# Kernel tuning notes

Measured on AMD Instinct MI355X. Metric: run time of the kernel, lower is better.

The kernel has to match this reference:

```python
import jax, jax.numpy as jnp
import numpy as np

IN_DIM = 128
OUT_DIM = 256
N_ETYPES = 4
N_STEPS = 8
B = 128
N_NODES = 256
E = 393216
CONCAT = IN_DIM + OUT_DIM


def _conv1d(x, w, b):
    # x: [B, C, L], w: [O, I, K] -> valid conv, stride 1
    y = jax.lax.conv_general_dilated(x, w, (1,), 'VALID', dimension_numbers=('NCH', 'OIH', 'NCH'))
    return y + b[None, :, None]


def _maxpool1d(x, k, s):
    return jax.lax.reduce_window(x, -jnp.inf, jax.lax.max, (1, 1, k), (1, 1, s), 'VALID')


def setup_inputs():
    key = jax.random.key(0)
    ks = jax.random.split(key, 16)
    Nn = B * N_NODES
    sc = 0.05
    f32 = jnp.float32
    return {
        'features': jax.random.normal(ks[0], (Nn, IN_DIM), f32),
        'src': jax.random.randint(ks[1], (E,), 0, Nn),
        'dst': jax.random.randint(ks[2], (E,), 0, Nn),
        'etype': jax.random.randint(ks[3], (E,), 0, N_ETYPES),
        'W_msg': jax.random.normal(ks[4], (N_ETYPES, OUT_DIM, OUT_DIM), f32) * sc,
        'b_msg': jnp.zeros((N_ETYPES, OUT_DIM), f32),
        'gru_Wi': jax.random.normal(ks[5], (OUT_DIM, 3 * OUT_DIM), f32) * sc,
        'gru_Wh': jax.random.normal(ks[6], (OUT_DIM, 3 * OUT_DIM), f32) * sc,
        'gru_bi': jnp.zeros((3 * OUT_DIM,), f32),
        'gru_bh': jnp.zeros((3 * OUT_DIM,), f32),
        'conv1_w': jax.random.normal(ks[7], (OUT_DIM, OUT_DIM, 3), f32) * sc,
        'conv1_b': jnp.zeros((OUT_DIM,), f32),
        'conv2_w': jax.random.normal(ks[8], (OUT_DIM, OUT_DIM, 1), f32) * sc,
        'conv2_b': jnp.zeros((OUT_DIM,), f32),
        'convc1_w': jax.random.normal(ks[9], (CONCAT, CONCAT, 3), f32) * sc,
        'convc1_b': jnp.zeros((CONCAT,), f32),
        'convc2_w': jax.random.normal(ks[10], (CONCAT, CONCAT, 1), f32) * sc,
        'convc2_b': jnp.zeros((CONCAT,), f32),
        'wy': jax.random.normal(ks[11], (OUT_DIM, 1), f32) * sc,
        'by': jnp.zeros((1,), f32),
        'wz': jax.random.normal(ks[12], (CONCAT, 1), f32) * sc,
        'bz': jnp.zeros((1,), f32),
        'num_graphs': B,
    }


def reference(features, src, dst, etype, W_msg, b_msg, gru_Wi, gru_Wh, gru_bi, gru_bh,
              conv1_w, conv1_b, conv2_w, conv2_b, convc1_w, convc1_b, convc2_w, convc2_b,
              wy, by, wz, bz, num_graphs):
    Nn = features.shape[0]
    # DGL GatedGraphConv: pad input feats up to out_feats
    h = jnp.pad(features, ((0, 0), (0, OUT_DIM - IN_DIM)))
    for _ in range(N_STEPS):
        # per-etype linear transform of all nodes: [Nn, T, O]
        H_all = jnp.einsum('nd,tdo->nto', h, W_msg) + b_msg[None]
        msg = H_all[src, etype]                              # [E, O]
        a = jax.ops.segment_sum(msg, dst, num_segments=Nn)   # [Nn, O]
        gi = a @ gru_Wi + gru_bi
        gh = h @ gru_Wh + gru_bh
        ir, iz, ig = jnp.split(gi, 3, axis=-1)
        hr, hz, hg = jnp.split(gh, 3, axis=-1)
        r = jax.nn.sigmoid(ir + hr)
        z = jax.nn.sigmoid(iz + hz)
        g = jnp.tanh(ig + r * hg)
        h = (1.0 - z) * g + z * h
    x_i = features.reshape(num_graphs, -1, IN_DIM)
    h_i = h.reshape(num_graphs, -1, OUT_DIM)
    c_i = jnp.concatenate([h_i, x_i], axis=-1)
    Y1 = _maxpool1d(jax.nn.relu(_conv1d(h_i.transpose(0, 2, 1), conv1_w, conv1_b)), 3, 2)
    Y2 = _maxpool1d(jax.nn.relu(_conv1d(Y1, conv2_w, conv2_b)), 2, 2).transpose(0, 2, 1)
    Z1 = _maxpool1d(jax.nn.relu(_conv1d(c_i.transpose(0, 2, 1), convc1_w, convc1_b)), 3, 2)
    Z2 = _maxpool1d(jax.nn.relu(_conv1d(Z1, convc2_w, convc2_b)), 2, 2).transpose(0, 2, 1)
    before_avg = (Y2 @ wy + by) * (Z2 @ wz + bz)   # [B, L, 1]
    avg = before_avg.mean(axis=1)                    # [B, 1]
    return jax.nn.sigmoid(avg).squeeze(-1)           # [B]
```

## Files before the change

kernel.cpp:

```cpp
#include <hip/hip_runtime.h>

#define DEV static __device__ __forceinline__

typedef float f32x4 __attribute__((ext_vector_type(4)));
typedef __bf16 bf16x8 __attribute__((ext_vector_type(8)));
typedef unsigned int u32x4 __attribute__((ext_vector_type(4)));
typedef unsigned int u32x2 __attribute__((ext_vector_type(2)));

#define NNODE 32768
#define NEDGE 393216

DEV unsigned short f2bf(float f) {
    unsigned int u = __builtin_bit_cast(unsigned int, f);
    u += 0x7FFFu + ((u >> 16) & 1u);
    return (unsigned short)(u >> 16);
}
DEV float bf2f(unsigned int b) {
    unsigned int u = b << 16;
    return __builtin_bit_cast(float, u);
}
DEV unsigned int pk2(float a, float b) {
    return (unsigned int)f2bf(a) | ((unsigned int)f2bf(b) << 16);
}
DEV float sigf(float x) { return 1.f / (1.f + __expf(-x)); }

DEV void gld16(const void* g, void* l) {
    __builtin_amdgcn_global_load_lds(
        (const __attribute__((address_space(1))) void*)(g),
        (__attribute__((address_space(3))) void*)(l),
        16, 0, 0);
}


__global__ __launch_bounds__(256) void init_k(
    const float* __restrict__ feat,
    unsigned short* __restrict__ hb0, unsigned short* __restrict__ hb1,
    unsigned short* __restrict__ fb)
{
    int idx = blockIdx.x * 256 + threadIdx.x;
    int r = idx >> 8, c = idx & 255;
    float f = 0.f;
    if (r < NNODE && c < 128) f = feat[(size_t)r * 128 + c];
    unsigned short v = f2bf(f);
    hb0[(size_t)r * 256 + c] = v;
    hb1[(size_t)r * 256 + c] = v;
    if (c < 128) fb[(size_t)r * 128 + c] = v;
}

__global__ __launch_bounds__(256) void prep_wmsg_k(
    const float* __restrict__ Wm, unsigned short* __restrict__ WT)
{
    int idx = blockIdx.x * 256 + threadIdx.x;
    int j = idx >> 8, d = idx & 255;
    int t = j >> 8, o = j & 255;
    WT[idx] = f2bf(Wm[t * 65536 + d * 256 + o]);
}

__global__ __launch_bounds__(256) void prep_gru_k(
    const float* __restrict__ Wi, const float* __restrict__ Wh,
    unsigned short* __restrict__ B2T)
{
    int idx = blockIdx.x * 256 + threadIdx.x;
    int j = idx >> 9, k = idx & 511;
    int band = j >> 6, g = (j >> 4) & 3, ch = (band << 4) + (j & 15);
    float v = 0.f;
    if (g == 0) v = (k < 256) ? Wi[k * 768 + ch] : Wh[(k - 256) * 768 + ch];
    else if (g == 1) v = (k < 256) ? Wi[k * 768 + 256 + ch] : Wh[(k - 256) * 768 + 256 + ch];
    else if (g == 2) { if (k < 256) v = Wi[k * 768 + 512 + ch]; }
    else { if (k >= 256) v = Wh[(k - 256) * 768 + 512 + ch]; }
    B2T[idx] = f2bf(v);
}

__global__ __launch_bounds__(256) void prep_bias2_k(
    const float* __restrict__ bi, const float* __restrict__ bh,
    float* __restrict__ b2)
{
    int j = blockIdx.x * 256 + threadIdx.x;
    int band = j >> 6, g = (j >> 4) & 3, ch = (band << 4) + (j & 15);
    float v;
    if (g == 0) v = bi[ch] + bh[ch];
    else if (g == 1) v = bi[256 + ch] + bh[256 + ch];
    else if (g == 2) v = bi[512 + ch];
    else v = bh[512 + ch];
    b2[j] = v;
}

__global__ __launch_bounds__(256) void prep_conv_k(
    const float* __restrict__ c1w, const float* __restrict__ c2w,
    const float* __restrict__ cc1w, const float* __restrict__ cc2w,
    unsigned short* __restrict__ BTY, unsigned short* __restrict__ BT2,
    unsigned short* __restrict__ BTZ, unsigned short* __restrict__ BTc2)
{
    int idx = blockIdx.x * 256 + threadIdx.x;
    if (idx < 196608) {
        int o = idx / 768, kk = idx - o * 768, k = kk >> 8, c = kk & 255;
        BTY[idx] = f2bf(c1w[o * 768 + c * 3 + k]);
    } else if (idx < 262144) {
        int r = idx - 196608, o = r >> 8, c = r & 255;
        BT2[r] = f2bf(c2w[o * 256 + c]);
    } else if (idx < 704512) {
        int jx = idx - 262144, o = jx / 1152, kk = jx - o * 1152;
        float v;
        if (kk < 768) { int k = kk >> 8, c = kk & 255; v = cc1w[o * 1152 + c * 3 + k]; }
        else { int r = kk - 768, kf = r >> 7, cf = r & 127; v = cc1w[o * 1152 + (256 + cf) * 3 + kf]; }
        BTZ[jx] = f2bf(v);
    } else {
        int r = idx - 704512, o = r / 384, c = r - o * 384;
        BTc2[r] = f2bf(cc2w[o * 384 + c]);
    }
}


__global__ __launch_bounds__(256) void count_k(
    const int* __restrict__ dst, int* __restrict__ cnt)
{
    int e = blockIdx.x * 256 + threadIdx.x;
    atomicAdd(&cnt[dst[e]], 1);
}

__global__ __launch_bounds__(1024) void scan1_k(
    const int* __restrict__ cnt, int* __restrict__ rp, int* __restrict__ bsum)
{
    __shared__ int buf[1024];
    int b = blockIdx.x, tid = threadIdx.x;
    int n = (b << 10) + tid;
    int v = cnt[n];
    buf[tid] = v;
    __syncthreads();
    for (int off = 1; off < 1024; off <<= 1) {
        int x = (tid >= off) ? buf[tid - off] : 0;
        __syncthreads();
        buf[tid] += x;
        __syncthreads();
    }
    rp[n] = buf[tid] - v;
    if (tid == 1023) bsum[b] = buf[1023];
}

__global__ __launch_bounds__(64) void scan2_k(
    const int* __restrict__ bsum, int* __restrict__ boff, int* __restrict__ rp)
{
    int lane = threadIdx.x;
    int v = (lane < 32) ? bsum[lane] : 0;
    int s = v;
    #pragma unroll
    for (int off = 1; off < 32; off <<= 1) {
        int x = __shfl_up(s, off, 64);
        if (lane >= off) s += x;
    }
    if (lane < 32) boff[lane] = s - v;
    if (lane == 31) rp[NNODE] = s;
}

__global__ __launch_bounds__(1024) void scan3_k(
    int* __restrict__ rp, const int* __restrict__ boff)
{
    int b = blockIdx.x, tid = threadIdx.x;
    rp[(b << 10) + tid] += boff[b];
}

__global__ __launch_bounds__(256) void fill_k(
    const int* __restrict__ src, const int* __restrict__ dst,
    const int* __restrict__ et, const int* __restrict__ rp,
    int* __restrict__ pos, int* __restrict__ edat)
{
    int e = blockIdx.x * 256 + threadIdx.x;
    int d = dst[e];
    int p = atomicAdd(&pos[d], 1);
    edat[rp[d] + p] = src[e] | (et[e] << 20);
}


__global__ __launch_bounds__(256) void agg2_k(
    const int* __restrict__ rp, const int* __restrict__ edat,
    const unsigned short* __restrict__ Hmsg, unsigned short* __restrict__ Aonly)
{
    int wave = threadIdx.x >> 6, lane = threadIdx.x & 63;
    int n = (blockIdx.x << 2) + wave;
    int e0 = rp[n], e1 = rp[n + 1];
    float a0 = 0.f, a1 = 0.f, a2 = 0.f, a3 = 0.f;
    const unsigned short* hc = Hmsg + (lane << 2);
    int e = e0;
    for (; e + 4 <= e1; e += 4) {
        int d0 = edat[e], d1 = edat[e + 1], d2 = edat[e + 2], d3 = edat[e + 3];
        u32x2 v0 = *(const u32x2*)(hc + ((size_t)(d0 & 0xFFFFF) << 10) + ((d0 >> 20) << 8));
        u32x2 v1 = *(const u32x2*)(hc + ((size_t)(d1 & 0xFFFFF) << 10) + ((d1 >> 20) << 8));
        u32x2 v2 = *(const u32x2*)(hc + ((size_t)(d2 & 0xFFFFF) << 10) + ((d2 >> 20) << 8));
        u32x2 v3 = *(const u32x2*)(hc + ((size_t)(d3 & 0xFFFFF) << 10) + ((d3 >> 20) << 8));
        a0 += bf2f(v0.x & 0xFFFFu) + bf2f(v1.x & 0xFFFFu) + bf2f(v2.x & 0xFFFFu) + bf2f(v3.x & 0xFFFFu);
        a1 += bf2f(v0.x >> 16) + bf2f(v1.x >> 16) + bf2f(v2.x >> 16) + bf2f(v3.x >> 16);
        a2 += bf2f(v0.y & 0xFFFFu) + bf2f(v1.y & 0xFFFFu) + bf2f(v2.y & 0xFFFFu) + bf2f(v3.y & 0xFFFFu);
        a3 += bf2f(v0.y >> 16) + bf2f(v1.y >> 16) + bf2f(v2.y >> 16) + bf2f(v3.y >> 16);
    }
    for (; e < e1; e++) {
        int d = edat[e];
        u32x2 v = *(const u32x2*)(hc + ((size_t)(d & 0xFFFFF) << 10) + ((d >> 20) << 8));
        a0 += bf2f(v.x & 0xFFFFu); a1 += bf2f(v.x >> 16);
        a2 += bf2f(v.y & 0xFFFFu); a3 += bf2f(v.y >> 16);
    }
    u32x2 p; p.x = pk2(a0, a1); p.y = pk2(a2, a3);
    *(u32x2*)(Aonly + (size_t)n * 256 + (lane << 2)) = p;
}

#define STAGE_COORDS                                            \
    int srow[4], scb[4], soff[4];                               \
    _Pragma("unroll")                                           \
    for (int p = 0; p < 4; p++) {                               \
        int c = wave + p * 4;                                   \
        int half = c >> 3, cc = c & 7;                          \
        srow[p] = cc * 16 + (lane >> 2);                        \
        scb[p] = ((lane & 3) + half * 4) * 8;                   \
        soff[p] = half * 4096 + cc * 512;                       \
    }

#define MFMA64(AS, BS)                                                        \
    _Pragma("unroll")                                                         \
    for (int h = 0; h < 2; h++) {                                             \
        bf16x8 af[4], bfr[4];                                                 \
        _Pragma("unroll")                                                     \
        for (int i = 0; i < 4; i++)                                           \
            af[i] = *(const bf16x8*)(&AS[h * 4096 + (qm + i * 16 + fm) * 32 + fkv * 8]); \
        _Pragma("unroll")                                                     \
        for (int i = 0; i < 4; i++)                                           \
            bfr[i] = *(const bf16x8*)(&BS[h * 4096 + (qn + i * 16 + fm) * 32 + fkv * 8]); \
        _Pragma("unroll")                                                     \
        for (int i = 0; i < 4; i++)                                           \
            _Pragma("unroll")                                                 \
            for (int j = 0; j < 4; j++)                                       \
                acc[i][j] = __builtin_amdgcn_mfma_f32_16x16x32_bf16(bfr[j], af[i], acc[i][j], 0, 0, 0); \
    }

__global__ __launch_bounds__(256) void gemm_bt(
    const unsigned short* __restrict__ A, int lda,
    const unsigned short* __restrict__ Bt,
    unsigned short* __restrict__ Cb, int ldcb,
    const float* __restrict__ bias,
    int N, int K, int swz, int relu)
{
    __shared__ __align__(16) unsigned short As[128 * 64];
    __shared__ __align__(16) unsigned short Bs[128 * 64];
    const int tid = threadIdx.x;
    int id = blockIdx.x;
    if (swz) { int per = gridDim.x >> 3; id = (id & 7) * per + (id >> 3); }
    const int nb = N >> 7;
    const int bm = id / nb, bn = id - bm * nb;
    const int wave = tid >> 6, lane = tid & 63;
    const unsigned short* Ag = A + (size_t)(bm * 128) * lda;
    const unsigned short* Bg = Bt + (size_t)(bn * 128) * K;
    const int qm = (wave & 1) << 6, qn = (wave >> 1) << 6;
    const int fm = lane & 15, fkv = lane >> 4;
    STAGE_COORDS

    f32x4 acc[4][4] = {};

    for (int kb = 0; kb < K; kb += 64) {
        __syncthreads();
        #pragma unroll
        for (int p = 0; p < 4; p++)
            gld16(Ag + (size_t)srow[p] * lda + kb + scb[p], As + soff[p]);
        #pragma unroll
        for (int p = 0; p < 4; p++)
            gld16(Bg + (size_t)srow[p] * K + kb + scb[p], Bs + soff[p]);
        __syncthreads();
        MFMA64(As, Bs)
    }

    const int m0 = bm * 128 + qm + fm;
    const int n0 = bn * 128 + qn + (fkv << 2);
    #pragma unroll
    for (int i = 0; i < 4; i++) {
        int row = m0 + i * 16;
        #pragma unroll
        for (int j = 0; j < 4; j++) {
            int col = n0 + j * 16;
            float v0 = acc[i][j][0], v1 = acc[i][j][1],
                  v2 = acc[i][j][2], v3 = acc[i][j][3];
            if (bias) {
                float4 bv = *(const float4*)(bias + col);
                v0 += bv.x; v1 += bv.y; v2 += bv.z; v3 += bv.w;
            }
            if (relu) {
                v0 = fmaxf(v0, 0.f); v1 = fmaxf(v1, 0.f);
                v2 = fmaxf(v2, 0.f); v3 = fmaxf(v3, 0.f);
            }
            u32x2 p; p.x = pk2(v0, v1); p.y = pk2(v2, v3);
            *(u32x2*)(Cb + (size_t)row * ldcb + col) = p;
        }
    }
}

__global__ __launch_bounds__(256) void gemm_conv(
    const unsigned short* __restrict__ Ah,
    const unsigned short* __restrict__ Af,
    const unsigned short* __restrict__ Bt,
    unsigned short* __restrict__ Cb, int ldcb,
    const float* __restrict__ bias,
    int N, int K)
{
    __shared__ __align__(16) unsigned short As[128 * 64];
    __shared__ __align__(16) unsigned short Bs[128 * 64];
    const int tid = threadIdx.x;
    int id = blockIdx.x;
    { int per = gridDim.x >> 3; id = (id & 7) * per + (id >> 3); }
    const int nb = N >> 7;
    const int bm = id / nb, bn = id - bm * nb;
    const int wave = tid >> 6, lane = tid & 63;
    const unsigned short* Bg = Bt + (size_t)(bn * 128) * K;
    const int qm = (wave & 1) << 6, qn = (wave >> 1) << 6;
    const int fm = lane & 15, fkv = lane >> 4;
    STAGE_COORDS

    f32x4 acc[4][4] = {};

    for (int kb = 0; kb < K; kb += 64) {
        const unsigned short* base; int ldA, col, shift;
        if (kb < 768) { base = Ah; ldA = 256; shift = kb >> 8; col = kb & 255; }
        else { int r = kb - 768; base = Af; ldA = 128; shift = r >> 7; col = r & 127; }
        const unsigned short* Ag = base + (size_t)(bm * 128 + shift) * ldA + col;
        __syncthreads();
        #pragma unroll
        for (int p = 0; p < 4; p++)
            gld16(Ag + (size_t)srow[p] * ldA + scb[p], As + soff[p]);
        #pragma unroll
        for (int p = 0; p < 4; p++)
            gld16(Bg + (size_t)srow[p] * K + kb + scb[p], Bs + soff[p]);
        __syncthreads();
        MFMA64(As, Bs)
    }

    const int m0 = bm * 128 + qm + fm;
    const int n0 = bn * 128 + qn + (fkv << 2);
    #pragma unroll
    for (int i = 0; i < 4; i++) {
        int row = m0 + i * 16;
        #pragma unroll
        for (int j = 0; j < 4; j++) {
            int col = n0 + j * 16;
            float4 bv = *(const float4*)(bias + col);
            float v0 = fmaxf(acc[i][j][0] + bv.x, 0.f);
            float v1 = fmaxf(acc[i][j][1] + bv.y, 0.f);
            float v2 = fmaxf(acc[i][j][2] + bv.z, 0.f);
            float v3 = fmaxf(acc[i][j][3] + bv.w, 0.f);
            u32x2 p; p.x = pk2(v0, v1); p.y = pk2(v2, v3);
            *(u32x2*)(Cb + (size_t)row * ldcb + col) = p;
        }
    }
}

__global__ __launch_bounds__(256) void gemm_gru(
    const unsigned short* __restrict__ Aonly,
    const unsigned short* __restrict__ hbc,
    const unsigned short* __restrict__ Bt,
    const float* __restrict__ b2p,
    unsigned short* __restrict__ hbn)
{
    __shared__ __align__(16) unsigned short As[128 * 64];
    __shared__ __align__(16) unsigned short Bs[128 * 64];
    const int tid = threadIdx.x;
    int id = blockIdx.x;
    { int per = gridDim.x >> 3; id = (id & 7) * per + (id >> 3); }
    const int bm = id >> 3;
    const int bn = id & 7;
    const int wave = tid >> 6, lane = tid & 63;
    const unsigned short* Bg = Bt + (size_t)(bn * 128) * 512;
    const int qm = (wave & 1) << 6, qn = (wave >> 1) << 6;
    const int fm = lane & 15, fkv = lane >> 4;
    STAGE_COORDS

    f32x4 acc[4][4] = {};

    #pragma unroll
    for (int kb = 0; kb < 512; kb += 64) {
        const unsigned short* base = (kb < 256) ? Aonly : hbc;
        const unsigned short* Ag = base + (size_t)(bm * 128) * 256 + (kb & 255);
        __syncthreads();
        #pragma unroll
        for (int p = 0; p < 4; p++)
            gld16(Ag + (size_t)srow[p] * 256 + scb[p], As + soff[p]);
        #pragma unroll
        for (int p = 0; p < 4; p++)
            gld16(Bg + (size_t)srow[p] * 512 + kb + scb[p], Bs + soff[p]);
        __syncthreads();
        MFMA64(As, Bs)
    }

    const int band = (bn << 1) + (qn >> 6);
    const int chb = (band << 4) + (fkv << 2);
    const float4 brv = *(const float4*)(b2p + (band << 6) + 0  + (fkv << 2));
    const float4 bzv = *(const float4*)(b2p + (band << 6) + 16 + (fkv << 2));
    const float4 bgv = *(const float4*)(b2p + (band << 6) + 32 + (fkv << 2));
    const float4 bhv = *(const float4*)(b2p + (band << 6) + 48 + (fkv << 2));
    const float br_[4] = {brv.x, brv.y, brv.z, brv.w};
    const float bz_[4] = {bzv.x, bzv.y, bzv.z, bzv.w};
    const float bg_[4] = {bgv.x, bgv.y, bgv.z, bgv.w};
    const float bh_[4] = {bhv.x, bhv.y, bhv.z, bhv.w};
    const int m0 = bm * 128 + qm + fm;
    #pragma unroll
    for (int i = 0; i < 4; i++) {
        int row = m0 + i * 16;
        u32x2 hv = *(const u32x2*)(hbc + (size_t)row * 256 + chb);
        float hp[4] = {bf2f(hv.x & 0xFFFFu), bf2f(hv.x >> 16),
                       bf2f(hv.y & 0xFFFFu), bf2f(hv.y >> 16)};
        float hn[4];
        #pragma unroll
        for (int r = 0; r < 4; r++) {
            float rg = sigf(acc[i][0][r] + br_[r]);
            float zz = sigf(acc[i][1][r] + bz_[r]);
            float pre = acc[i][2][r] + bg_[r] + rg * (acc[i][3][r] + bh_[r]);
            pre = fminf(fmaxf(pre, -15.f), 15.f);
            float t = __expf(2.f * pre);
            float gq = (t - 1.f) / (t + 1.f);
            hn[r] = (1.f - zz) * gq + zz * hp[r];
        }
        u32x2 p; p.x = pk2(hn[0], hn[1]); p.y = pk2(hn[2], hn[3]);
        *(u32x2*)(hbn + (size_t)row * 256 + chb) = p;
    }
}

__global__ __launch_bounds__(256) void pool_k(
    const unsigned short* __restrict__ in, int ldin, int Lb_in, int L_out,
    int win, int C,
    unsigned short* __restrict__ ob, float* __restrict__ of, int ldo)
{
    int idx = blockIdx.x * 256 + threadIdx.x;
    int c = idx % C;
    int row = idx / C;
    int b = row / L_out, lp = row - b * L_out;
    const unsigned short* p = in + (size_t)(b * Lb_in + 2 * lp) * ldin + c;
    float m = bf2f(p[0]);
    for (int d = 1; d < win; d++) m = fmaxf(m, bf2f(p[(size_t)d * ldin]));
    if (ob) ob[(size_t)row * ldo + c] = f2bf(m);
    else    of[(size_t)row * ldo + c] = m;
}

__global__ __launch_bounds__(64) void final_k(
    const float* __restrict__ Y2, const float* __restrict__ Z2,
    const float* __restrict__ wy, const float* __restrict__ by,
    const float* __restrict__ wz, const float* __restrict__ bz,
    float* __restrict__ out)
{
    int b = blockIdx.x, lane = threadIdx.x;
    float val = 0.f;
    if (lane < 63) {
        const float* yr = Y2 + (size_t)(b * 63 + lane) * 256;
        float y = 0.f;
        for (int o = 0; o < 256; o += 4) {
            float4 a = *(const float4*)(yr + o);
            float4 wv = *(const float4*)(wy + o);
            y += a.x * wv.x + a.y * wv.y + a.z * wv.z + a.w * wv.w;
        }
        y += by[0];
        const float* zr = Z2 + (size_t)(b * 63 + lane) * 384;
        float z = 0.f;
        for (int o = 0; o < 384; o += 4) {
            float4 a = *(const float4*)(zr + o);
            float4 wv = *(const float4*)(wz + o);
            z += a.x * wv.x + a.y * wv.y + a.z * wv.z + a.w * wv.w;
        }
        z += bz[0];
        val = y * z;
    }
    for (int off = 32; off > 0; off >>= 1) val += __shfl_down(val, off, 64);
    if (lane == 0) out[b] = sigf(val * (1.f / 63.f));
}


extern "C" void kernel_launch(void* const* d_in, const int* in_sizes, int n_in,
                              void* d_out, int out_size, void* d_ws, size_t ws_size,
                              hipStream_t stream)
{
    const float* feat = (const float*)d_in[0];
    const int* src = (const int*)d_in[1];
    const int* dst = (const int*)d_in[2];
    const int* et  = (const int*)d_in[3];
    const float* Wm  = (const float*)d_in[4];
    const float* bm  = (const float*)d_in[5];
    const float* Wi  = (const float*)d_in[6];
    const float* Wh  = (const float*)d_in[7];
    const float* bi  = (const float*)d_in[8];
    const float* bh  = (const float*)d_in[9];
    const float* c1w = (const float*)d_in[10];
    const float* c1b = (const float*)d_in[11];
    const float* c2w = (const float*)d_in[12];
    const float* c2b = (const float*)d_in[13];
    const float* cc1w = (const float*)d_in[14];
    const float* cc1b = (const float*)d_in[15];
    const float* cc2w = (const float*)d_in[16];
    const float* cc2b = (const float*)d_in[17];
    const float* wy = (const float*)d_in[18];
    const float* by = (const float*)d_in[19];
    const float* wz = (const float*)d_in[20];
    const float* bz = (const float*)d_in[21];
    float* out = (float*)d_out;

    char* w = (char*)d_ws;
    size_t off = 0;
    auto alloc = [&](size_t bytes) -> char* {
        char* p = w + off; off += (bytes + 255) & ~(size_t)255; return p;
    };
    unsigned short* hb0 = (unsigned short*)alloc((size_t)(NNODE + 8) * 256 * 2);
    unsigned short* hb1 = (unsigned short*)alloc((size_t)(NNODE + 8) * 256 * 2);
    unsigned short* fb  = (unsigned short*)alloc((size_t)(NNODE + 8) * 128 * 2);
    unsigned short* Aonly = (unsigned short*)alloc((size_t)NNODE * 256 * 2);
    char* R = alloc((size_t)NNODE * 1024 * 2);
    unsigned short* Hmsg = (unsigned short*)R;
    unsigned short* CbY  = (unsigned short*)R;
    unsigned short* CbZ  = (unsigned short*)(R + (size_t)NNODE * 256 * 2);
    unsigned short* P    = (unsigned short*)alloc((size_t)16128 * 384 * 2);
    unsigned short* Cb2  = (unsigned short*)alloc((size_t)16128 * 384 * 2);
    float* Y2 = (float*)alloc((size_t)8064 * 256 * 4);
    float* Z2 = (float*)alloc((size_t)8064 * 384 * 4);
    unsigned short* WT   = (unsigned short*)alloc(1024 * 256 * 2);
    unsigned short* B2T  = (unsigned short*)alloc(1024 * 512 * 2);
    float* b2            = (float*)alloc(1024 * 4);
    unsigned short* BTY  = (unsigned short*)alloc(256 * 768 * 2);
    unsigned short* BT2  = (unsigned short*)alloc(256 * 256 * 2);
    unsigned short* BTZ  = (unsigned short*)alloc(384 * 1152 * 2);
    unsigned short* BTc2 = (unsigned short*)alloc(384 * 384 * 2);
    int* rp     = (int*)alloc((NNODE + 1) * 4);
    int* pos    = (int*)alloc(NNODE * 4);
    int* cnt    = (int*)alloc(NNODE * 4);
    int* bsum   = (int*)alloc(32 * 4);
    int* boff   = (int*)alloc(32 * 4);
    int* edat   = (int*)alloc(NEDGE * 4);

    hipLaunchKernelGGL(init_k, dim3(NNODE + 8), dim3(256), 0, stream, feat, hb0, hb1, fb);
    hipLaunchKernelGGL(prep_wmsg_k, dim3(1024), dim3(256), 0, stream, Wm, WT);
    hipLaunchKernelGGL(prep_gru_k, dim3(2048), dim3(256), 0, stream, Wi, Wh, B2T);
    hipLaunchKernelGGL(prep_bias2_k, dim3(4), dim3(256), 0, stream, bi, bh, b2);
    hipLaunchKernelGGL(prep_conv_k, dim3(3328), dim3(256), 0, stream,
                       c1w, c2w, cc1w, cc2w, BTY, BT2, BTZ, BTc2);
    hipMemsetAsync(pos, 0, NNODE * 4, stream);
    hipMemsetAsync(cnt, 0, NNODE * 4, stream);
    hipLaunchKernelGGL(count_k, dim3(NEDGE / 256), dim3(256), 0, stream, dst, cnt);
    hipLaunchKernelGGL(scan1_k, dim3(32), dim3(1024), 0, stream, cnt, rp, bsum);
    hipLaunchKernelGGL(scan2_k, dim3(1), dim3(64), 0, stream, bsum, boff, rp);
    hipLaunchKernelGGL(scan3_k, dim3(32), dim3(1024), 0, stream, rp, boff);
    hipLaunchKernelGGL(fill_k, dim3(NEDGE / 256), dim3(256), 0, stream, src, dst, et, rp, pos, edat);

    unsigned short* hbuf[2] = {hb0, hb1};
    for (int step = 0; step < 8; step++) {
        unsigned short* cur = hbuf[step & 1];
        unsigned short* nxt = hbuf[(step + 1) & 1];
        hipLaunchKernelGGL(gemm_bt, dim3(2048), dim3(256), 0, stream,
            cur, 256, WT, Hmsg, 1024, bm, 1024, 256, 1, 0);
        hipLaunchKernelGGL(agg2_k, dim3(NNODE / 4), dim3(256), 0, stream, rp, edat, Hmsg, Aonly);
        hipLaunchKernelGGL(gemm_gru, dim3(2048), dim3(256), 0, stream,
            Aonly, cur, B2T, b2, nxt);
    }

    hipLaunchKernelGGL(gemm_conv, dim3(512), dim3(256), 0, stream,
        hb0, (const unsigned short*)nullptr, BTY, CbY, 256, c1b, 256, 768);
    hipLaunchKernelGGL(pool_k, dim3(16128), dim3(256), 0, stream,
        CbY, 256, 256, 126, 3, 256, P, (float*)nullptr, 256);
    hipLaunchKernelGGL(gemm_bt, dim3(252), dim3(256), 0, stream,
        P, 256, BT2, Cb2, 256, c2b, 256, 256, 0, 1);
    hipLaunchKernelGGL(pool_k, dim3(8064), dim3(256), 0, stream,
        Cb2, 256, 126, 63, 2, 256, (unsigned short*)nullptr, Y2, 256);

    hipLaunchKernelGGL(gemm_conv, dim3(768), dim3(256), 0, stream,
        hb0, fb, BTZ, CbZ, 384, cc1b, 384, 1152);
    hipLaunchKernelGGL(pool_k, dim3(24192), dim3(256), 0, stream,
        CbZ, 384, 256, 126, 3, 384, P, (float*)nullptr, 384);
    hipLaunchKernelGGL(gemm_bt, dim3(378), dim3(256), 0, stream,
        P, 384, BTc2, Cb2, 384, cc2b, 384, 384, 0, 1);
    hipLaunchKernelGGL(pool_k, dim3(12096), dim3(256), 0, stream,
        Cb2, 384, 126, 63, 2, 384, (unsigned short*)nullptr, Z2, 384);

    hipLaunchKernelGGL(final_k, dim3(128), dim3(64), 0, stream, Y2, Z2, wy, by, wz, bz, out);
}
```

Before: 1.334 ms.

## Load GEMM B fragments directly to registers, fuse final pool, deepen gather unroll

All three MFMA GEMM kernels now load their B-operand fragments straight from global memory into registers instead of staging them through shared memory. This halves LDS usage and removes the B-side LDS traffic, but it issues uncoalesced 16-byte global loads per lane with no reuse across waves. The final 2-wide max-pool is folded into final_k, which reads the bf16 conv2 outputs directly, so two pool kernel launches and their fp32 intermediate buffers go away. The edge aggregation loop is unrolled from 4 to 8 independent gathers to keep more loads in flight.

```diff
diff --git a/kernel.cpp b/kernel.cpp
--- a/kernel.cpp
+++ b/kernel.cpp
@@ -181,16 +181,18 @@
     float a0 = 0.f, a1 = 0.f, a2 = 0.f, a3 = 0.f;
     const unsigned short* hc = Hmsg + (lane << 2);
     int e = e0;
-    for (; e + 4 <= e1; e += 4) {
-        int d0 = edat[e], d1 = edat[e + 1], d2 = edat[e + 2], d3 = edat[e + 3];
-        u32x2 v0 = *(const u32x2*)(hc + ((size_t)(d0 & 0xFFFFF) << 10) + ((d0 >> 20) << 8));
-        u32x2 v1 = *(const u32x2*)(hc + ((size_t)(d1 & 0xFFFFF) << 10) + ((d1 >> 20) << 8));
-        u32x2 v2 = *(const u32x2*)(hc + ((size_t)(d2 & 0xFFFFF) << 10) + ((d2 >> 20) << 8));
-        u32x2 v3 = *(const u32x2*)(hc + ((size_t)(d3 & 0xFFFFF) << 10) + ((d3 >> 20) << 8));
-        a0 += bf2f(v0.x & 0xFFFFu) + bf2f(v1.x & 0xFFFFu) + bf2f(v2.x & 0xFFFFu) + bf2f(v3.x & 0xFFFFu);
-        a1 += bf2f(v0.x >> 16) + bf2f(v1.x >> 16) + bf2f(v2.x >> 16) + bf2f(v3.x >> 16);
-        a2 += bf2f(v0.y & 0xFFFFu) + bf2f(v1.y & 0xFFFFu) + bf2f(v2.y & 0xFFFFu) + bf2f(v3.y & 0xFFFFu);
-        a3 += bf2f(v0.y >> 16) + bf2f(v1.y >> 16) + bf2f(v2.y >> 16) + bf2f(v3.y >> 16);
+    for (; e + 8 <= e1; e += 8) {
+        u32x2 v[8];
+        #pragma unroll
+        for (int q = 0; q < 8; q++) {
+            int d = edat[e + q];
+            v[q] = *(const u32x2*)(hc + ((size_t)(d & 0xFFFFF) << 10) + ((d >> 20) << 8));
+        }
+        #pragma unroll
+        for (int q = 0; q < 8; q++) {
+            a0 += bf2f(v[q].x & 0xFFFFu); a1 += bf2f(v[q].x >> 16);
+            a2 += bf2f(v[q].y & 0xFFFFu); a3 += bf2f(v[q].y >> 16);
+        }
     }
     for (; e < e1; e++) {
         int d = edat[e];
@@ -213,21 +215,18 @@
         soff[p] = half * 4096 + cc * 512;                       \
     }
 
-#define MFMA64(AS, BS)                                                        \
+#define MFMA64_BD(AS, BREG)                                                   \
     _Pragma("unroll")                                                         \
     for (int h = 0; h < 2; h++) {                                             \
-        bf16x8 af[4], bfr[4];                                                 \
+        bf16x8 af[4];                                                         \
         _Pragma("unroll")                                                     \
         for (int i = 0; i < 4; i++)                                           \
             af[i] = *(const bf16x8*)(&AS[h * 4096 + (qm + i * 16 + fm) * 32 + fkv * 8]); \
         _Pragma("unroll")                                                     \
         for (int i = 0; i < 4; i++)                                           \
-            bfr[i] = *(const bf16x8*)(&BS[h * 4096 + (qn + i * 16 + fm) * 32 + fkv * 8]); \
-        _Pragma("unroll")                                                     \
-        for (int i = 0; i < 4; i++)                                           \
             _Pragma("unroll")                                                 \
             for (int j = 0; j < 4; j++)                                       \
-                acc[i][j] = __builtin_amdgcn_mfma_f32_16x16x32_bf16(bfr[j], af[i], acc[i][j], 0, 0, 0); \
+                acc[i][j] = __builtin_amdgcn_mfma_f32_16x16x32_bf16(BREG[h][j], af[i], acc[i][j], 0, 0, 0); \
     }
 
 __global__ __launch_bounds__(256) void gemm_bt(
@@ -238,7 +237,6 @@
     int N, int K, int swz, int relu)
 {
     __shared__ __align__(16) unsigned short As[128 * 64];
-    __shared__ __align__(16) unsigned short Bs[128 * 64];
     const int tid = threadIdx.x;
     int id = blockIdx.x;
     if (swz) { int per = gridDim.x >> 3; id = (id & 7) * per + (id >> 3); }
@@ -246,23 +244,26 @@
     const int bm = id / nb, bn = id - bm * nb;
     const int wave = tid >> 6, lane = tid & 63;
     const unsigned short* Ag = A + (size_t)(bm * 128) * lda;
-    const unsigned short* Bg = Bt + (size_t)(bn * 128) * K;
     const int qm = (wave & 1) << 6, qn = (wave >> 1) << 6;
     const int fm = lane & 15, fkv = lane >> 4;
+    const unsigned short* Bf = Bt + (size_t)(bn * 128 + qn + fm) * K + fkv * 8;
     STAGE_COORDS
 
     f32x4 acc[4][4] = {};
 
     for (int kb = 0; kb < K; kb += 64) {
+        bf16x8 breg[2][4];
+        #pragma unroll
+        for (int h = 0; h < 2; h++)
+            #pragma unroll
+            for (int j = 0; j < 4; j++)
+                breg[h][j] = *(const bf16x8*)(Bf + (size_t)j * 16 * K + kb + h * 32);
         __syncthreads();
         #pragma unroll
         for (int p = 0; p < 4; p++)
             gld16(Ag + (size_t)srow[p] * lda + kb + scb[p], As + soff[p]);
-        #pragma unroll
-        for (int p = 0; p < 4; p++)
-            gld16(Bg + (size_t)srow[p] * K + kb + scb[p], Bs + soff[p]);
-        __syncthreads();
-        MFMA64(As, Bs)
+        __syncthreads();
+        MFMA64_BD(As, breg)
     }
 
     const int m0 = bm * 128 + qm + fm;
@@ -298,21 +299,26 @@
     int N, int K)
 {
     __shared__ __align__(16) unsigned short As[128 * 64];
-    __shared__ __align__(16) unsigned short Bs[128 * 64];
     const int tid = threadIdx.x;
     int id = blockIdx.x;
     { int per = gridDim.x >> 3; id = (id & 7) * per + (id >> 3); }
     const int nb = N >> 7;
     const int bm = id / nb, bn = id - bm * nb;
     const int wave = tid >> 6, lane = tid & 63;
-    const unsigned short* Bg = Bt + (size_t)(bn * 128) * K;
     const int qm = (wave & 1) << 6, qn = (wave >> 1) << 6;
     const int fm = lane & 15, fkv = lane >> 4;
+    const unsigned short* Bf = Bt + (size_t)(bn * 128 + qn + fm) * K + fkv * 8;
     STAGE_COORDS
 
     f32x4 acc[4][4] = {};
 
     for (int kb = 0; kb < K; kb += 64) {
+        bf16x8 breg[2][4];
+        #pragma unroll
+        for (int h = 0; h < 2; h++)
+            #pragma unroll
+            for (int j = 0; j < 4; j++)
+                breg[h][j] = *(const bf16x8*)(Bf + (size_t)j * 16 * K + kb + h * 32);
         const unsigned short* base; int ldA, col, shift;
         if (kb < 768) { base = Ah; ldA = 256; shift = kb >> 8; col = kb & 255; }
         else { int r = kb - 768; base = Af; ldA = 128; shift = r >> 7; col = r & 127; }
@@ -321,11 +327,8 @@
         #pragma unroll
         for (int p = 0; p < 4; p++)
             gld16(Ag + (size_t)srow[p] * ldA + scb[p], As + soff[p]);
-        #pragma unroll
-        for (int p = 0; p < 4; p++)
-            gld16(Bg + (size_t)srow[p] * K + kb + scb[p], Bs + soff[p]);
-        __syncthreads();
-        MFMA64(As, Bs)
+        __syncthreads();
+        MFMA64_BD(As, breg)
     }
 
     const int m0 = bm * 128 + qm + fm;
@@ -355,33 +358,34 @@
     unsigned short* __restrict__ hbn)
 {
     __shared__ __align__(16) unsigned short As[128 * 64];
-    __shared__ __align__(16) unsigned short Bs[128 * 64];
     const int tid = threadIdx.x;
     int id = blockIdx.x;
     { int per = gridDim.x >> 3; id = (id & 7) * per + (id >> 3); }
     const int bm = id >> 3;
     const int bn = id & 7;
     const int wave = tid >> 6, lane = tid & 63;
-    const unsigned short* Bg = Bt + (size_t)(bn * 128) * 512;
     const int qm = (wave & 1) << 6, qn = (wave >> 1) << 6;
     const int fm = lane & 15, fkv = lane >> 4;
+    const unsigned short* Bf = Bt + (size_t)(bn * 128 + qn + fm) * 512 + fkv * 8;
     STAGE_COORDS
 
     f32x4 acc[4][4] = {};
 
-    #pragma unroll
     for (int kb = 0; kb < 512; kb += 64) {
+        bf16x8 breg[2][4];
+        #pragma unroll
+        for (int h = 0; h < 2; h++)
+            #pragma unroll
+            for (int j = 0; j < 4; j++)
+                breg[h][j] = *(const bf16x8*)(Bf + (size_t)j * 16 * 512 + kb + h * 32);
         const unsigned short* base = (kb < 256) ? Aonly : hbc;
         const unsigned short* Ag = base + (size_t)(bm * 128) * 256 + (kb & 255);
         __syncthreads();
         #pragma unroll
         for (int p = 0; p < 4; p++)
             gld16(Ag + (size_t)srow[p] * 256 + scb[p], As + soff[p]);
-        #pragma unroll
-        for (int p = 0; p < 4; p++)
-            gld16(Bg + (size_t)srow[p] * 512 + kb + scb[p], Bs + soff[p]);
-        __syncthreads();
-        MFMA64(As, Bs)
+        __syncthreads();
+        MFMA64_BD(As, breg)
     }
 
     const int band = (bn << 1) + (qn >> 6);
@@ -420,7 +424,7 @@
 __global__ __launch_bounds__(256) void pool_k(
     const unsigned short* __restrict__ in, int ldin, int Lb_in, int L_out,
     int win, int C,
-    unsigned short* __restrict__ ob, float* __restrict__ of, int ldo)
+    unsigned short* __restrict__ ob, int ldo)
 {
     int idx = blockIdx.x * 256 + threadIdx.x;
     int c = idx % C;
@@ -429,12 +433,11 @@
     const unsigned short* p = in + (size_t)(b * Lb_in + 2 * lp) * ldin + c;
     float m = bf2f(p[0]);
     for (int d = 1; d < win; d++) m = fmaxf(m, bf2f(p[(size_t)d * ldin]));
-    if (ob) ob[(size_t)row * ldo + c] = f2bf(m);
-    else    of[(size_t)row * ldo + c] = m;
+    ob[(size_t)row * ldo + c] = f2bf(m);
 }
 
 __global__ __launch_bounds__(64) void final_k(
-    const float* __restrict__ Y2, const float* __restrict__ Z2,
+    const unsigned short* __restrict__ CY, const unsigned short* __restrict__ CZ,
     const float* __restrict__ wy, const float* __restrict__ by,
     const float* __restrict__ wz, const float* __restrict__ bz,
     float* __restrict__ out)
@@ -442,21 +445,17 @@
     int b = blockIdx.x, lane = threadIdx.x;
     float val = 0.f;
     if (lane < 63) {
-        const float* yr = Y2 + (size_t)(b * 63 + lane) * 256;
+        const unsigned short* y0 = CY + (size_t)(b * 126 + 2 * lane) * 256;
+        const unsigned short* y1 = y0 + 256;
         float y = 0.f;
-        for (int o = 0; o < 256; o += 4) {
-            float4 a = *(const float4*)(yr + o);
-            float4 wv = *(const float4*)(wy + o);
-            y += a.x * wv.x + a.y * wv.y + a.z * wv.z + a.w * wv.w;
-        }
+        for (int o = 0; o < 256; o++)
+            y += fmaxf(bf2f(y0[o]), bf2f(y1[o])) * wy[o];
         y += by[0];
-        const float* zr = Z2 + (size_t)(b * 63 + lane) * 384;
+        const unsigned short* z0 = CZ + (size_t)(b * 126 + 2 * lane) * 384;
+        const unsigned short* z1 = z0 + 384;
         float z = 0.f;
-        for (int o = 0; o < 384; o += 4) {
-            float4 a = *(const float4*)(zr + o);
-            float4 wv = *(const float4*)(wz + o);
-            z += a.x * wv.x + a.y * wv.y + a.z * wv.z + a.w * wv.w;
-        }
+        for (int o = 0; o < 384; o++)
+            z += fmaxf(bf2f(z0[o]), bf2f(z1[o])) * wz[o];
         z += bz[0];
         val = y * z;
     }
@@ -507,9 +506,8 @@
     unsigned short* CbY  = (unsigned short*)R;
     unsigned short* CbZ  = (unsigned short*)(R + (size_t)NNODE * 256 * 2);
     unsigned short* P    = (unsigned short*)alloc((size_t)16128 * 384 * 2);
-    unsigned short* Cb2  = (unsigned short*)alloc((size_t)16128 * 384 * 2);
-    float* Y2 = (float*)alloc((size_t)8064 * 256 * 4);
-    float* Z2 = (float*)alloc((size_t)8064 * 384 * 4);
+    unsigned short* Cb2Y = (unsigned short*)alloc((size_t)16128 * 256 * 2);
+    unsigned short* Cb2Z = (unsigned short*)alloc((size_t)16128 * 384 * 2);
     unsigned short* WT   = (unsigned short*)alloc(1024 * 256 * 2);
     unsigned short* B2T  = (unsigned short*)alloc(1024 * 512 * 2);
     float* b2            = (float*)alloc(1024 * 4);
@@ -552,20 +550,17 @@
     hipLaunchKernelGGL(gemm_conv, dim3(512), dim3(256), 0, stream,
         hb0, (const unsigned short*)nullptr, BTY, CbY, 256, c1b, 256, 768);
     hipLaunchKernelGGL(pool_k, dim3(16128), dim3(256), 0, stream,
-        CbY, 256, 256, 126, 3, 256, P, (float*)nullptr, 256);
+        CbY, 256, 256, 126, 3, 256, P, 256);
     hipLaunchKernelGGL(gemm_bt, dim3(252), dim3(256), 0, stream,
-        P, 256, BT2, Cb2, 256, c2b, 256, 256, 0, 1);
-    hipLaunchKernelGGL(pool_k, dim3(8064), dim3(256), 0, stream,
-        Cb2, 256, 126, 63, 2, 256, (unsigned short*)nullptr, Y2, 256);
+        P, 256, BT2, Cb2Y, 256, c2b, 256, 256, 0, 1);
 
     hipLaunchKernelGGL(gemm_conv, dim3(768), dim3(256), 0, stream,
         hb0, fb, BTZ, CbZ, 384, cc1b, 384, 1152);
     hipLaunchKernelGGL(pool_k, dim3(24192), dim3(256), 0, stream,
-        CbZ, 384, 256, 126, 3, 384, P, (float*)nullptr, 384);
+        CbZ, 384, 256, 126, 3, 384, P, 384);
     hipLaunchKernelGGL(gemm_bt, dim3(378), dim3(256), 0, stream,
-        P, 384, BTc2, Cb2, 384, cc2b, 384, 384, 0, 1);
-    hipLaunchKernelGGL(pool_k, dim3(12096), dim3(256), 0, stream,
-        Cb2, 384, 126, 63, 2, 384, (unsigned short*)nullptr, Z2, 384);
-
-    hipLaunchKernelGGL(final_k, dim3(128), dim3(64), 0, stream, Y2, Z2, wy, by, wz, bz, out);
-}
+        P, 384, BTc2, Cb2Z, 384, cc2b, 384, 384, 0, 1);
+
+    hipLaunchKernelGGL(final_k, dim3(128), dim3(64), 0, stream,
+        Cb2Y, Cb2Z, wy, by, wz, bz, out);
+}
```

New measurement: 1.715 ms. +28.6%, slower.
